# Performance work log

Measured on AMD Instinct MI355X. Metric: run time of the kernel, lower is better.

## Reference

```python
import jax, jax.numpy as jnp
import numpy as np
from jax import lax

D, H, DH, F, K, L, N = 512, 8, 64, 2048, 31, 512, 16
EPS = 1e-5

def layer_norm(x, g, b):
    m = x.mean(-1, keepdims=True)
    v = ((x - m) ** 2).mean(-1, keepdims=True)
    return (x - m) / jnp.sqrt(v + EPS) * g + b

def swish(x):
    return x * jax.nn.sigmoid(x)

def ffn(x, w1, b1, w2, b2):
    return swish(x @ w1.T + b1) @ w2.T + b2

def rel_shift(x):
    # x: (N,H,T,2T-1) -> (N,H,T,T); out[...,i,j] = x[...,i, T-1-i+j]
    T = x.shape[2]
    rows = jnp.arange(T)[:, None]
    cols = (T - 1) - rows + jnp.arange(T)[None, :]
    return x[:, :, rows, cols]

def rel_attn(x, pos_emb, in_w, in_b, out_w, out_b, pos_w, bu, bv):
    Lq, Nb, E = x.shape
    qkv = x @ in_w.T + in_b  # (L,N,3E)
    q, k, v = jnp.split(qkv, 3, axis=-1)
    q = q.reshape(Lq, Nb, H, DH).transpose(1, 2, 0, 3)  # (N,H,L,DH)
    k = k.reshape(Lq, Nb, H, DH).transpose(1, 2, 0, 3)
    v = v.reshape(Lq, Nb, H, DH).transpose(1, 2, 0, 3)
    p = (pos_emb[0] @ pos_w.T).reshape(-1, H, DH).transpose(1, 0, 2)  # (H,2L-1,DH)
    scaling = DH ** -0.5
    q_u = q + bu[None, :, None, :]
    q_v = q + bv[None, :, None, :]
    matrix_ac = jnp.einsum('nhld,nhsd->nhls', q_u, k)        # (N,H,L,L)
    matrix_bd = jnp.einsum('nhld,hmd->nhlm', q_v, p)         # (N,H,L,2L-1)
    matrix_bd = rel_shift(matrix_bd)                         # (N,H,L,L)
    attn = jax.nn.softmax((matrix_ac + matrix_bd) * scaling, axis=-1)
    out = jnp.einsum('nhls,nhsd->nhld', attn, v)
    out = out.transpose(2, 0, 1, 3).reshape(Lq, Nb, E)
    return out @ out_w.T + out_b

def conv_module(x, pw1_w, pw1_b, dw_w, dw_b, g, b, mean, var, pw2_w, pw2_b):
    # x: (L,N,C) -> (N,C,L)
    y = x.transpose(1, 2, 0)
    y = jnp.einsum('ncl,oc->nol', y, pw1_w) + pw1_b[None, :, None]
    a, gate = jnp.split(y, 2, axis=1)
    y = a * jax.nn.sigmoid(gate)  # GLU over channel dim
    pad = (K - 1) // 2
    y = lax.conv_general_dilated(y, dw_w[:, None, :], (1,), [(pad, pad)],
                                 feature_group_count=D,
                                 dimension_numbers=('NCH', 'OIH', 'NCH'))
    y = y + dw_b[None, :, None]
    # BatchNorm1d in eval mode with running stats
    y = (y - mean[None, :, None]) / jnp.sqrt(var[None, :, None] + EPS)
    y = y * g[None, :, None] + b[None, :, None]
    y = swish(y)
    y = jnp.einsum('ncl,oc->nol', y, pw2_w) + pw2_b[None, :, None]
    return y.transpose(2, 0, 1)  # back to (L,N,C)

def setup_inputs() -> dict:
    key = jax.random.key(0)
    ks = iter(jax.random.split(key, 64))
    def nrm(shape, s=0.02):
        return jax.random.normal(next(ks), shape, dtype=jnp.float32) * s
    return {
        'src': jax.random.normal(next(ks), (L, N, D), dtype=jnp.float32),
        'pos_emb': jax.random.normal(next(ks), (1, 2 * L - 1, D), dtype=jnp.float32),
        'ffm_w1': nrm((F, D)), 'ffm_b1': jnp.zeros((F,), jnp.float32),
        'ffm_w2': nrm((D, F)), 'ffm_b2': jnp.zeros((D,), jnp.float32),
        'ff_w1': nrm((F, D)), 'ff_b1': jnp.zeros((F,), jnp.float32),
        'ff_w2': nrm((D, F)), 'ff_b2': jnp.zeros((D,), jnp.float32),
        'in_proj_w': nrm((3 * D, D)), 'in_proj_b': jnp.zeros((3 * D,), jnp.float32),
        'out_proj_w': nrm((D, D)), 'out_proj_b': jnp.zeros((D,), jnp.float32),
        'pos_w': nrm((D, D)),
        'pos_bias_u': nrm((H, DH)), 'pos_bias_v': nrm((H, DH)),
        'conv_pw1_w': nrm((2 * D, D)), 'conv_pw1_b': jnp.zeros((2 * D,), jnp.float32),
        'conv_dw_w': nrm((D, K)), 'conv_dw_b': jnp.zeros((D,), jnp.float32),
        'bn_gamma': jnp.ones((D,), jnp.float32), 'bn_beta': jnp.zeros((D,), jnp.float32),
        'bn_mean': jnp.zeros((D,), jnp.float32), 'bn_var': jnp.ones((D,), jnp.float32),
        'conv_pw2_w': nrm((D, D)), 'conv_pw2_b': jnp.zeros((D,), jnp.float32),
        'ln_ffm_g': jnp.ones((D,), jnp.float32), 'ln_ffm_b': jnp.zeros((D,), jnp.float32),
        'ln_mha_g': jnp.ones((D,), jnp.float32), 'ln_mha_b': jnp.zeros((D,), jnp.float32),
        'ln_conv_g': jnp.ones((D,), jnp.float32), 'ln_conv_b': jnp.zeros((D,), jnp.float32),
        'ln_ff_g': jnp.ones((D,), jnp.float32), 'ln_ff_b': jnp.zeros((D,), jnp.float32),
        'ln_final_g': jnp.ones((D,), jnp.float32), 'ln_final_b': jnp.zeros((D,), jnp.float32),
    }

def reference(src, pos_emb, ffm_w1, ffm_b1, ffm_w2, ffm_b2, ff_w1, ff_b1, ff_w2, ff_b2,
              in_proj_w, in_proj_b, out_proj_w, out_proj_b, pos_w, pos_bias_u, pos_bias_v,
              conv_pw1_w, conv_pw1_b, conv_dw_w, conv_dw_b, bn_gamma, bn_beta, bn_mean, bn_var,
              conv_pw2_w, conv_pw2_b, ln_ffm_g, ln_ffm_b, ln_mha_g, ln_mha_b, ln_conv_g, ln_conv_b,
              ln_ff_g, ln_ff_b, ln_final_g, ln_final_b):
    # pre-norm conformer block, ff_scale = 0.5, dropout omitted (eval)
    x = src
    x = x + 0.5 * ffn(layer_norm(x, ln_ffm_g, ln_ffm_b), ffm_w1, ffm_b1, ffm_w2, ffm_b2)
    x = x + rel_attn(layer_norm(x, ln_mha_g, ln_mha_b), pos_emb,
                     in_proj_w, in_proj_b, out_proj_w, out_proj_b,
                     pos_w, pos_bias_u, pos_bias_v)
    x = x + conv_module(layer_norm(x, ln_conv_g, ln_conv_b),
                        conv_pw1_w, conv_pw1_b, conv_dw_w, conv_dw_b,
                        bn_gamma, bn_beta, bn_mean, bn_var, conv_pw2_w, conv_pw2_b)
    x = x + 0.5 * ffn(layer_norm(x, ln_ff_g, ln_ff_b), ff_w1, ff_b1, ff_w2, ff_b2)
    return layer_norm(x, ln_final_g, ln_final_b)
```

## Files before the change

### kernel.cpp

```cpp
#include <hip/hip_runtime.h>
#include <cstdint>
#include <cstddef>

typedef unsigned short u16;
typedef __attribute__((ext_vector_type(4))) float f32x4;
typedef __attribute__((ext_vector_type(8))) short bf16x8;
typedef __attribute__((ext_vector_type(8))) unsigned short u16x8;

__device__ __forceinline__ float sigm(float x) { return 1.f / (1.f + __expf(-x)); }
__device__ __forceinline__ float bf2f(u16 u) {
    union { unsigned int i; float f; } c; c.i = ((unsigned int)u) << 16; return c.f;
}
__device__ __forceinline__ u16 f2bf(float f) {
    union { float f; unsigned int i; } c; c.f = f;
    unsigned int x = c.i;
    x += 0x7fffu + ((x >> 16) & 1u);
    return (u16)(x >> 16);
}


__global__ void castall_k(const float* __restrict__ s0, const float* __restrict__ s1,
                          const float* __restrict__ s2, const float* __restrict__ s3,
                          const float* __restrict__ s4, const float* __restrict__ s5,
                          const float* __restrict__ s6, const float* __restrict__ s7,
                          const float* __restrict__ s8, const float* __restrict__ s9,
                          u16* __restrict__ dst) {
    int i = blockIdx.x * 256 + threadIdx.x;
    if (i >= 6815232) return;
    const float* s; int off;
    if      (i < 1048576) { s = s0; off = 0; }
    else if (i < 2097152) { s = s1; off = 1048576; }
    else if (i < 3145728) { s = s2; off = 2097152; }
    else if (i < 4194304) { s = s3; off = 3145728; }
    else if (i < 4980736) { s = s4; off = 4194304; }
    else if (i < 5242880) { s = s5; off = 4980736; }
    else if (i < 5767168) { s = s6; off = 5242880; }
    else if (i < 6029312) { s = s7; off = 5767168; }
    else if (i < 6291456) { s = s8; off = 6029312; }
    else                  { s = s9; off = 6291456; }
    dst[i] = f2bf(s[i - off]);
}

template <bool OUTBF>
__global__ __launch_bounds__(256) void ln512_k(const float* __restrict__ x,
                                               const float* __restrict__ g,
                                               const float* __restrict__ b,
                                               void* __restrict__ outv) {
    int row = blockIdx.x * 4 + (threadIdx.x >> 6);
    int lane = threadIdx.x & 63;
    const float* xr = x + (size_t)row * 512 + lane * 8;
    float4 v0 = *(const float4*)(xr);
    float4 v1 = *(const float4*)(xr + 4);
    float va[8] = {v0.x, v0.y, v0.z, v0.w, v1.x, v1.y, v1.z, v1.w};
    float s = 0.f;
#pragma unroll
    for (int t = 0; t < 8; t++) s += va[t];
#pragma unroll
    for (int o = 32; o > 0; o >>= 1) s += __shfl_xor(s, o);
    float m = s * (1.0f / 512.0f);
    float q = 0.f;
#pragma unroll
    for (int t = 0; t < 8; t++) { float d = va[t] - m; q += d * d; }
#pragma unroll
    for (int o = 32; o > 0; o >>= 1) q += __shfl_xor(q, o);
    float inv = rsqrtf(q * (1.0f / 512.0f) + 1e-5f);
    int cb = lane * 8;
    if (OUTBF) {
        u16* o = (u16*)outv + (size_t)row * 512 + cb;
#pragma unroll
        for (int t = 0; t < 8; t++)
            o[t] = f2bf((va[t] - m) * inv * g[cb + t] + b[cb + t]);
    } else {
        float* o = (float*)outv + (size_t)row * 512 + cb;
#pragma unroll
        for (int t = 0; t < 8; t++)
            o[t] = (va[t] - m) * inv * g[cb + t] + b[cb + t];
    }
}

__global__ __launch_bounds__(256) void mgemm_k(
    const u16* __restrict__ A, const u16* __restrict__ B, const float* __restrict__ bias,
    const float* __restrict__ add, void* __restrict__ Cv,
    int M, int Nn, int Kk, float coef, int act, int outbf) {
    __shared__ u16 lA[2][4096];
    __shared__ u16 lB[2][4096];
    int tid = threadIdx.x;
    int lane = tid & 63;
    int w = tid >> 6;
    int wm = (w >> 1) * 64, wn = (w & 1) * 64;
    int m0 = blockIdx.x << 7, n0 = blockIdx.y << 7;

    f32x4 acc[4][4];
#pragma unroll
    for (int i = 0; i < 4; i++)
#pragma unroll
        for (int j = 0; j < 4; j++) acc[i][j] = (f32x4){0.f, 0.f, 0.f, 0.f};

    int srow = tid >> 2;
    int scol = (tid & 3) << 3;
    const u16* gA = A + (size_t)(m0 + srow) * Kk + scol;
    const u16* gB = B + (size_t)(n0 + srow) * Kk + scol;
    int lso = tid * 8;
    int lra = wm * 32 + (lane & 15) * 32 + (lane >> 4) * 8;
    int lrb = wn * 32 + (lane & 15) * 32 + (lane >> 4) * 8;

    auto STAGE = [&](int buf, int k0) {
        __builtin_amdgcn_global_load_lds(
            (const __attribute__((address_space(1))) void*)(gA + k0),
            (__attribute__((address_space(3))) void*)(lA[buf] + lso), 16, 0, 0);
        __builtin_amdgcn_global_load_lds(
            (const __attribute__((address_space(1))) void*)(gA + (size_t)64 * Kk + k0),
            (__attribute__((address_space(3))) void*)(lA[buf] + 2048 + lso), 16, 0, 0);
        __builtin_amdgcn_global_load_lds(
            (const __attribute__((address_space(1))) void*)(gB + k0),
            (__attribute__((address_space(3))) void*)(lB[buf] + lso), 16, 0, 0);
        __builtin_amdgcn_global_load_lds(
            (const __attribute__((address_space(1))) void*)(gB + (size_t)64 * Kk + k0),
            (__attribute__((address_space(3))) void*)(lB[buf] + 2048 + lso), 16, 0, 0);
    };
    auto COMP = [&](int buf) {
        bf16x8 af[4], bf[4];
#pragma unroll
        for (int t = 0; t < 4; t++) {
            af[t] = *(const bf16x8*)(lA[buf] + lra + t * 512);
            bf[t] = *(const bf16x8*)(lB[buf] + lrb + t * 512);
        }
#pragma unroll
        for (int i = 0; i < 4; i++)
#pragma unroll
            for (int j = 0; j < 4; j++)
                acc[i][j] = __builtin_amdgcn_mfma_f32_16x16x32_bf16(af[i], bf[j], acc[i][j], 0, 0, 0);
    };

    int nk = Kk >> 5;
    STAGE(0, 0);
    __syncthreads();
    for (int kt = 1; kt < nk; kt++) {
        STAGE(kt & 1, kt << 5);
        COMP((kt - 1) & 1);
        __syncthreads();
    }
    COMP((nk - 1) & 1);

    int rbase = (lane >> 4) * 4;
    int ncol = lane & 15;
#pragma unroll
    for (int i = 0; i < 4; i++) {
#pragma unroll
        for (int j = 0; j < 4; j++) {
            int n = n0 + wn + j * 16 + ncol;
            float bv = bias ? bias[n] : 0.f;
#pragma unroll
            for (int r = 0; r < 4; r++) {
                int m = m0 + wm + i * 16 + rbase + r;
                float c = acc[i][j][r] + bv;
                if (act == 1) c *= sigm(c);
                size_t o = (size_t)m * Nn + n;
                if (add) c = add[o] + coef * c;
                if (outbf) ((u16*)Cv)[o] = f2bf(c);
                else ((float*)Cv)[o] = c;
            }
        }
    }
}

__global__ __launch_bounds__(256) void posb_k(const u16* __restrict__ A,
                                              const u16* __restrict__ B,
                                              u16* __restrict__ Pbf) {
    __shared__ u16 lA[4096];
    __shared__ u16 lB[4096];
    const int Kk = 512;
    int tid = threadIdx.x;
    int lane = tid & 63, w = tid >> 6;
    int wm = (w >> 1) * 64, wn = (w & 1) * 64;
    int m0 = blockIdx.x << 7, n0 = blockIdx.y << 7;

    f32x4 acc[4][4];
#pragma unroll
    for (int i = 0; i < 4; i++)
#pragma unroll
        for (int j = 0; j < 4; j++) acc[i][j] = (f32x4){0.f, 0.f, 0.f, 0.f};

    int srow = tid >> 2;
    int scol = (tid & 3) << 3;
    int ar0 = m0 + srow;       if (ar0 > 1022) ar0 = 1022;
    int ar1 = m0 + 64 + srow;  if (ar1 > 1022) ar1 = 1022;
    const u16* gA0 = A + (size_t)ar0 * Kk + scol;
    const u16* gA1 = A + (size_t)ar1 * Kk + scol;
    const u16* gB = B + (size_t)(n0 + srow) * Kk + scol;
    int lso = tid * 8;
    int lra = wm * 32 + (lane & 15) * 32 + (lane >> 4) * 8;
    int lrb = wn * 32 + (lane & 15) * 32 + (lane >> 4) * 8;

    for (int k0 = 0; k0 < Kk; k0 += 32) {
        __builtin_amdgcn_global_load_lds(
            (const __attribute__((address_space(1))) void*)(gA0 + k0),
            (__attribute__((address_space(3))) void*)(lA + lso), 16, 0, 0);
        __builtin_amdgcn_global_load_lds(
            (const __attribute__((address_space(1))) void*)(gA1 + k0),
            (__attribute__((address_space(3))) void*)(lA + 2048 + lso), 16, 0, 0);
        __builtin_amdgcn_global_load_lds(
            (const __attribute__((address_space(1))) void*)(gB + k0),
            (__attribute__((address_space(3))) void*)(lB + lso), 16, 0, 0);
        __builtin_amdgcn_global_load_lds(
            (const __attribute__((address_space(1))) void*)(gB + (size_t)64 * Kk + k0),
            (__attribute__((address_space(3))) void*)(lB + 2048 + lso), 16, 0, 0);
        __syncthreads();
        bf16x8 af[4], bf[4];
#pragma unroll
        for (int t = 0; t < 4; t++) {
            af[t] = *(const bf16x8*)(lA + lra + t * 512);
            bf[t] = *(const bf16x8*)(lB + lrb + t * 512);
        }
#pragma unroll
        for (int i = 0; i < 4; i++)
#pragma unroll
            for (int j = 0; j < 4; j++)
                acc[i][j] = __builtin_amdgcn_mfma_f32_16x16x32_bf16(af[i], bf[j], acc[i][j], 0, 0, 0);
        __syncthreads();
    }

    int rbase = (lane >> 4) * 4;
    int ncol = lane & 15;
#pragma unroll
    for (int i = 0; i < 4; i++) {
#pragma unroll
        for (int j = 0; j < 4; j++) {
            int n = n0 + wn + j * 16 + ncol;
            int h = n >> 6, d = n & 63;
#pragma unroll
            for (int r = 0; r < 4; r++) {
                int m = m0 + wm + i * 16 + rbase + r;
                u16 val = (m < 1023) ? f2bf(acc[i][j][r]) : (u16)0;
                Pbf[(((size_t)(h * 1024 + m)) << 6) + d] = val;
            }
        }
    }
}

__global__ __launch_bounds__(256) void fattn_k(
    const u16* __restrict__ QU, const u16* __restrict__ QV,
    const u16* __restrict__ Kb, const u16* __restrict__ Pbf,
    const u16* __restrict__ VT, u16* __restrict__ ctx) {
    __shared__ u16 arr[19072];
    u16* sRect = arr;
    u16* sP = arr;
    u16* sCtx = arr + 16768;
    float* sRed = (float*)(arr + 18816);

    int tid = threadIdx.x;
    int lane = tid & 63, w = tid >> 6;
    int quad = lane >> 4, col = lane & 15;
    int nh = blockIdx.x, h = nh & 7, nb = nh >> 3;
    int m0 = blockIdx.y << 5;
    int nlo = 480 - m0;

    const u16* QVz = QV + ((size_t)nh << 15);
    const u16* QUz = QU + ((size_t)nh << 15);
    const u16* Kz  = Kb + ((size_t)nh << 15);
    const u16* Vz  = VT + ((size_t)nh << 15);
    const u16* Pb  = Pbf + ((size_t)h << 16);

    bf16x8 av[2][2];
#pragma unroll
    for (int ks = 0; ks < 2; ks++)
#pragma unroll
        for (int t = 0; t < 2; t++)
            av[ks][t] = *(const bf16x8*)(QVz + ((size_t)(m0 + t * 16 + col) << 6) + (ks << 5) + quad * 8);
#pragma unroll
    for (int idx = 0; idx < 9; idx++) {
        int nt = w + (idx << 2);
        if (nt < 34) {
            int crow = nt * 16 + col;
            const u16* pb = Pb + ((size_t)(nlo + crow) << 6) + quad * 8;
            f32x4 b0 = (f32x4){0.f, 0.f, 0.f, 0.f};
            f32x4 b1 = (f32x4){0.f, 0.f, 0.f, 0.f};
#pragma unroll
            for (int ks = 0; ks < 2; ks++) {
                bf16x8 bfr = *(const bf16x8*)(pb + (ks << 5));
                b0 = __builtin_amdgcn_mfma_f32_16x16x32_bf16(av[ks][0], bfr, b0, 0, 0, 0);
                b1 = __builtin_amdgcn_mfma_f32_16x16x32_bf16(av[ks][1], bfr, b1, 0, 0, 0);
            }
#pragma unroll
            for (int r = 0; r < 4; r++) {
                int ml0 = quad * 4 + r;
                int j0 = crow + ml0 - 31;
                if (j0 >= 0 && j0 < 512) sRect[ml0 * 524 + j0] = f2bf(b0[r]);
                int ml1 = ml0 + 16;
                int j1 = crow + ml1 - 31;
                if (j1 >= 0 && j1 < 512) sRect[ml1 * 524 + j1] = f2bf(b1[r]);
            }
        }
    }

    bf16x8 au[2][2];
#pragma unroll
    for (int ks = 0; ks < 2; ks++)
#pragma unroll
        for (int t = 0; t < 2; t++)
            au[ks][t] = *(const bf16x8*)(QUz + ((size_t)(m0 + t * 16 + col) << 6) + (ks << 5) + quad * 8);
    f32x4 ac[2][8];
#pragma unroll
    for (int t = 0; t < 2; t++)
#pragma unroll
        for (int jt = 0; jt < 8; jt++) ac[t][jt] = (f32x4){0.f, 0.f, 0.f, 0.f};
#pragma unroll
    for (int jt = 0; jt < 8; jt++) {
        const u16* kp = Kz + ((size_t)((w << 7) + jt * 16 + col) << 6) + quad * 8;
#pragma unroll
        for (int ks = 0; ks < 2; ks++) {
            bf16x8 bfr = *(const bf16x8*)(kp + (ks << 5));
            ac[0][jt] = __builtin_amdgcn_mfma_f32_16x16x32_bf16(au[ks][0], bfr, ac[0][jt], 0, 0, 0);
            ac[1][jt] = __builtin_amdgcn_mfma_f32_16x16x32_bf16(au[ks][1], bfr, ac[1][jt], 0, 0, 0);
        }
    }
    __syncthreads();

    float rmax[2][4];
#pragma unroll
    for (int t = 0; t < 2; t++)
#pragma unroll
        for (int r = 0; r < 4; r++) rmax[t][r] = -1e30f;
#pragma unroll
    for (int jt = 0; jt < 8; jt++) {
        int j = (w << 7) + jt * 16 + col;
#pragma unroll
        for (int t = 0; t < 2; t++)
#pragma unroll
            for (int r = 0; r < 4; r++) {
                int ml = t * 16 + quad * 4 + r;
                float v = (ac[t][jt][r] + bf2f(sRect[ml * 524 + j])) * 0.125f;
                ac[t][jt][r] = v;
                rmax[t][r] = fmaxf(rmax[t][r], v);
            }
    }
#pragma unroll
    for (int o = 1; o <= 8; o <<= 1)
#pragma unroll
        for (int t = 0; t < 2; t++)
#pragma unroll
            for (int r = 0; r < 4; r++) rmax[t][r] = fmaxf(rmax[t][r], __shfl_xor(rmax[t][r], o));
    if (col == 0)
#pragma unroll
        for (int t = 0; t < 2; t++)
#pragma unroll
            for (int r = 0; r < 4; r++) sRed[(t * 16 + quad * 4 + r) * 4 + w] = rmax[t][r];
    __syncthreads();
    float gmax[2][4], psum[2][4];
#pragma unroll
    for (int t = 0; t < 2; t++)
#pragma unroll
        for (int r = 0; r < 4; r++) {
            int ml = t * 16 + quad * 4 + r;
            gmax[t][r] = fmaxf(fmaxf(sRed[ml * 4 + 0], sRed[ml * 4 + 1]),
                               fmaxf(sRed[ml * 4 + 2], sRed[ml * 4 + 3]));
            psum[t][r] = 0.f;
        }
    __syncthreads();
#pragma unroll
    for (int jt = 0; jt < 8; jt++)
#pragma unroll
        for (int t = 0; t < 2; t++)
#pragma unroll
            for (int r = 0; r < 4; r++) {
                float e = __expf(ac[t][jt][r] - gmax[t][r]);
                ac[t][jt][r] = e;
                psum[t][r] += e;
            }
#pragma unroll
    for (int o = 1; o <= 8; o <<= 1)
#pragma unroll
        for (int t = 0; t < 2; t++)
#pragma unroll
            for (int r = 0; r < 4; r++) psum[t][r] += __shfl_xor(psum[t][r], o);
    if (col == 0)
#pragma unroll
        for (int t = 0; t < 2; t++)
#pragma unroll
            for (int r = 0; r < 4; r++) sRed[(t * 16 + quad * 4 + r) * 4 + w] = psum[t][r];
    __syncthreads();
    float rinv[2][4];
#pragma unroll
    for (int t = 0; t < 2; t++)
#pragma unroll
        for (int r = 0; r < 4; r++) {
            int ml = t * 16 + quad * 4 + r;
            rinv[t][r] = 1.f / (sRed[ml * 4 + 0] + sRed[ml * 4 + 1] + sRed[ml * 4 + 2] + sRed[ml * 4 + 3]);
        }

#pragma unroll
    for (int jt = 0; jt < 8; jt++) {
        int j = (w << 7) + jt * 16 + col;
#pragma unroll
        for (int t = 0; t < 2; t++)
#pragma unroll
            for (int r = 0; r < 4; r++)
                sP[(t * 16 + quad * 4 + r) * 520 + j] = f2bf(ac[t][jt][r] * rinv[t][r]);
    }
    __syncthreads();

    f32x4 cacc[2];
    cacc[0] = (f32x4){0.f, 0.f, 0.f, 0.f};
    cacc[1] = (f32x4){0.f, 0.f, 0.f, 0.f};
    {
        const u16* vp = Vz + ((size_t)((w << 4) + col) << 9) + quad * 8;
#pragma unroll
        for (int kc = 0; kc < 2; kc++)
#pragma unroll
            for (int s2 = 0; s2 < 8; s2++) {
                int ko = (kc << 8) + (s2 << 5);
                bf16x8 a0 = *(const bf16x8*)(sP + col * 520 + ko + quad * 8);
                bf16x8 a1 = *(const bf16x8*)(sP + (col + 16) * 520 + ko + quad * 8);
                bf16x8 bfr = *(const bf16x8*)(vp + ko);
                cacc[0] = __builtin_amdgcn_mfma_f32_16x16x32_bf16(a0, bfr, cacc[0], 0, 0, 0);
                cacc[1] = __builtin_amdgcn_mfma_f32_16x16x32_bf16(a1, bfr, cacc[1], 0, 0, 0);
            }
    }

#pragma unroll
    for (int t = 0; t < 2; t++)
#pragma unroll
        for (int r = 0; r < 4; r++)
            sCtx[(t * 16 + quad * 4 + r) * 64 + (w << 4) + col] = f2bf(cacc[t][r]);
    __syncthreads();
    {
        int row = tid >> 3, seg = tid & 7;
        u16* dst = ctx + (((size_t)((m0 + row) * 16 + nb)) << 9) + (h << 6) + seg * 8;
        *(uint4*)dst = *(const uint4*)(sCtx + row * 64 + seg * 8);
    }
}

__global__ __launch_bounds__(256) void repack_k(const u16* __restrict__ qkv,
                                                const float* __restrict__ bu,
                                                const float* __restrict__ bv,
                                                u16* __restrict__ QU, u16* __restrict__ QV,
                                                u16* __restrict__ Kb, u16* __restrict__ VT) {
    __shared__ u16 sV[64 * 72];
    int nh = blockIdx.x, h = nh & 7, n = nh >> 3;
    int l0 = blockIdx.y << 6;
    int tid = threadIdx.x;
    int d8 = (tid & 7) << 3;
    float bub[8], bvb[8];
#pragma unroll
    for (int e = 0; e < 8; e++) {
        bub[e] = bu[h * 64 + d8 + e];
        bvb[e] = bv[h * 64 + d8 + e];
    }
#pragma unroll
    for (int rep = 0; rep < 2; rep++) {
        int ll = (tid >> 3) + rep * 32;
        int l = l0 + ll;
        size_t base = (size_t)(l * 16 + n) * 1536 + h * 64 + d8;
        u16x8 q = *(const u16x8*)(qkv + base);
        u16x8 k = *(const u16x8*)(qkv + base + 512);
        u16x8 v = *(const u16x8*)(qkv + base + 1024);
        u16x8 qu, qv;
#pragma unroll
        for (int e = 0; e < 8; e++) {
            float qf = bf2f(q[e]);
            qu[e] = f2bf(qf + bub[e]);
            qv[e] = f2bf(qf + bvb[e]);
        }
        size_t o = ((size_t)nh * 512 + l) * 64 + d8;
        *(u16x8*)(QU + o) = qu;
        *(u16x8*)(QV + o) = qv;
        *(u16x8*)(Kb + o) = k;
        *(u16x8*)(sV + ll * 72 + d8) = v;
    }
    __syncthreads();
    int d = tid >> 2, ls = (tid & 3) << 4;
    u16 tmp[16];
#pragma unroll
    for (int e = 0; e < 16; e++) tmp[e] = sV[(ls + e) * 72 + d];
    u16* dst = VT + ((size_t)nh * 64 + d) * 512 + l0 + ls;
    *(u16x8*)(dst) = *(const u16x8*)(tmp);
    *(u16x8*)(dst + 8) = *(const u16x8*)(tmp + 8);
}

__global__ void glu_k(const u16* __restrict__ pw1o, u16* __restrict__ g) {
    int e = blockIdx.x * 256 + threadIdx.x;
    int t = e >> 9, c = e & 511;
    float a = bf2f(pw1o[(size_t)t * 1024 + c]);
    float ga = bf2f(pw1o[(size_t)t * 1024 + 512 + c]);
    g[e] = f2bf(a * sigm(ga));
}

__global__ __launch_bounds__(256) void dwconv_k(
    const u16* __restrict__ g, const float* __restrict__ w, const float* __restrict__ wb,
    const float* __restrict__ bng, const float* __restrict__ bnb, const float* __restrict__ bnm,
    const float* __restrict__ bnv, u16* __restrict__ out) {
    int idx = blockIdx.x * 256 + threadIdx.x;
    int c = idx & 511;
    int t = idx >> 9;
    int n = t & 15, l0 = (t >> 4) << 4;
    float win[46];
#pragma unroll
    for (int q = 0; q < 46; q++) {
        int ll = l0 - 15 + q;
        win[q] = (ll >= 0 && ll < 512) ? bf2f(g[((size_t)(ll * 16 + n) << 9) + c]) : 0.f;
    }
    float wgt[31];
#pragma unroll
    for (int k = 0; k < 31; k++) wgt[k] = w[c * 31 + k];
    float ivg = rsqrtf(bnv[c] + 1e-5f) * bng[c];
    float mc = bnm[c], bc = bnb[c], wbc = wb[c];
#pragma unroll
    for (int r = 0; r < 16; r++) {
        float acc = 0.f;
#pragma unroll
        for (int k = 0; k < 31; k++) acc += wgt[k] * win[r + k];
        acc += wbc;
        float y = (acc - mc) * ivg + bc;
        y = y * sigm(y);
        out[((size_t)((l0 + r) * 16 + n) << 9) + c] = f2bf(y);
    }
}

extern "C" void kernel_launch(void* const* d_in, const int* in_sizes, int n_in,
                              void* d_out, int out_size, void* d_ws, size_t ws_size,
                              hipStream_t stream) {
    const float* src      = (const float*)d_in[0];
    const float* pos_emb  = (const float*)d_in[1];
    const float* ffm_w1   = (const float*)d_in[2];
    const float* ffm_b1   = (const float*)d_in[3];
    const float* ffm_w2   = (const float*)d_in[4];
    const float* ffm_b2   = (const float*)d_in[5];
    const float* ff_w1    = (const float*)d_in[6];
    const float* ff_b1    = (const float*)d_in[7];
    const float* ff_w2    = (const float*)d_in[8];
    const float* ff_b2    = (const float*)d_in[9];
    const float* in_w     = (const float*)d_in[10];
    const float* in_b     = (const float*)d_in[11];
    const float* out_w    = (const float*)d_in[12];
    const float* out_b    = (const float*)d_in[13];
    const float* pos_w    = (const float*)d_in[14];
    const float* bu       = (const float*)d_in[15];
    const float* bv       = (const float*)d_in[16];
    const float* pw1_w    = (const float*)d_in[17];
    const float* pw1_b    = (const float*)d_in[18];
    const float* dw_w     = (const float*)d_in[19];
    const float* dw_b     = (const float*)d_in[20];
    const float* bng      = (const float*)d_in[21];
    const float* bnb      = (const float*)d_in[22];
    const float* bnm      = (const float*)d_in[23];
    const float* bnv      = (const float*)d_in[24];
    const float* pw2_w    = (const float*)d_in[25];
    const float* pw2_b    = (const float*)d_in[26];
    const float* ln_ffm_g = (const float*)d_in[27];
    const float* ln_ffm_b = (const float*)d_in[28];
    const float* ln_mha_g = (const float*)d_in[29];
    const float* ln_mha_b = (const float*)d_in[30];
    const float* ln_cv_g  = (const float*)d_in[31];
    const float* ln_cv_b  = (const float*)d_in[32];
    const float* ln_ff_g  = (const float*)d_in[33];
    const float* ln_ff_b  = (const float*)d_in[34];
    const float* ln_fin_g = (const float*)d_in[35];
    const float* ln_fin_b = (const float*)d_in[36];
    (void)in_sizes; (void)n_in; (void)out_size; (void)ws_size;

    const size_t MEG = 1048576;
    u16* U = (u16*)d_ws;
    float* xA = (float*)U;
    u16* Pbf = U;
    float* xB = (float*)(U + 8 * MEG);
    u16* LNB = U + 16 * MEG;
    u16* BIG = U + 20 * MEG;
    u16* QU = U + 36 * MEG;
    u16* QV = U + 40 * MEG;
    u16* Kb = U + 44 * MEG;
    u16* VT = U + 48 * MEG;
    u16* WB = U + 52 * MEG;
    u16* w_ffm1 = WB;
    u16* w_ffm2 = WB + 1 * MEG;
    u16* w_ff1  = WB + 2 * MEG;
    u16* w_ff2  = WB + 3 * MEG;
    u16* w_in   = WB + 4 * MEG;
    u16* w_out  = WB + 4 * MEG + 786432;
    u16* w_pw1  = WB + 5 * MEG;
    u16* w_pw2  = WB + 5 * MEG + 524288;
    u16* w_pos  = WB + 6029312;
    u16* w_pe   = WB + 6291456;
    u16* CTX = LNB;
    u16* GLU = QU;
    u16* CACT = QV;

    castall_k<<<26622, 256, 0, stream>>>(ffm_w1, ffm_w2, ff_w1, ff_w2, in_w, out_w,
                                         pw1_w, pw2_w, pos_w, pos_emb, WB);

    ln512_k<true><<<2048, 256, 0, stream>>>(src, ln_ffm_g, ln_ffm_b, LNB);
    mgemm_k<<<dim3(64, 16), 256, 0, stream>>>(LNB, w_ffm1, ffm_b1, nullptr, BIG,
                                              8192, 2048, 512, 0.f, 1, 1);
    mgemm_k<<<dim3(64, 4), 256, 0, stream>>>(BIG, w_ffm2, ffm_b2, src, xB,
                                             8192, 512, 2048, 0.5f, 0, 0);

    ln512_k<true><<<2048, 256, 0, stream>>>(xB, ln_mha_g, ln_mha_b, LNB);
    posb_k<<<dim3(8, 4), 256, 0, stream>>>(w_pe, w_pos, Pbf);
    mgemm_k<<<dim3(64, 12), 256, 0, stream>>>(LNB, w_in, in_b, nullptr, BIG,
                                              8192, 1536, 512, 0.f, 0, 1);
    repack_k<<<dim3(128, 8), 256, 0, stream>>>(BIG, bu, bv, QU, QV, Kb, VT);
    fattn_k<<<dim3(128, 16), 256, 0, stream>>>(QU, QV, Kb, Pbf, VT, CTX);
    mgemm_k<<<dim3(64, 4), 256, 0, stream>>>(CTX, w_out, out_b, xB, xA,
                                             8192, 512, 512, 1.f, 0, 0);

    ln512_k<true><<<2048, 256, 0, stream>>>(xA, ln_cv_g, ln_cv_b, LNB);
    mgemm_k<<<dim3(64, 8), 256, 0, stream>>>(LNB, w_pw1, pw1_b, nullptr, BIG,
                                             8192, 1024, 512, 0.f, 0, 1);
    glu_k<<<16384, 256, 0, stream>>>(BIG, GLU);
    dwconv_k<<<1024, 256, 0, stream>>>(GLU, dw_w, dw_b, bng, bnb, bnm, bnv, CACT);
    mgemm_k<<<dim3(64, 4), 256, 0, stream>>>(CACT, w_pw2, pw2_b, xA, xB,
                                             8192, 512, 512, 1.f, 0, 0);

    ln512_k<true><<<2048, 256, 0, stream>>>(xB, ln_ff_g, ln_ff_b, LNB);
    mgemm_k<<<dim3(64, 16), 256, 0, stream>>>(LNB, w_ff1, ff_b1, nullptr, BIG,
                                              8192, 2048, 512, 0.f, 1, 1);
    mgemm_k<<<dim3(64, 4), 256, 0, stream>>>(BIG, w_ff2, ff_b2, xB, xA,
                                             8192, 512, 2048, 0.5f, 0, 0);

    ln512_k<false><<<2048, 256, 0, stream>>>(xA, ln_fin_g, ln_fin_b, (float*)d_out);
}
```

Before: 607.5 us.

## Add 256x256-tile GEMM with direct-to-LDS loads for wide projections

Adds a new 512-thread GEMM kernel with 256x256 output tiles, double-buffered 64-wide K slices loaded straight into LDS via global_load_lds with an XOR swizzle, and 16x16x32 bf16 MFMA. It is used for the four wide-N projections (FFN up-projections, QKV in-projection, pointwise conv 1). The larger tile is meant to raise operand reuse and cut global traffic per FLOP. The cost is 128KB of LDS per block and far fewer blocks (128–256 on 256 CUs), which risks low occupancy and poor CU fill.

```diff
diff --git a/kernel.cpp b/kernel.cpp
--- a/kernel.cpp
+++ b/kernel.cpp
@@ -75,6 +75,108 @@
 #pragma unroll
         for (int t = 0; t < 8; t++)
             o[t] = (va[t] - m) * inv * g[cb + t] + b[cb + t];
+    }
+}
+
+__global__ __launch_bounds__(512, 2) void mgemm256_k(
+    const u16* __restrict__ A, const u16* __restrict__ B, const float* __restrict__ bias,
+    const float* __restrict__ add, void* __restrict__ Cv,
+    int M, int Nn, int Kk, float coef, int act, int outbf) {
+    __shared__ u16 sh[65536];
+    int tid = threadIdx.x;
+    int lane = tid & 63, w = tid >> 6;
+    int quad = lane >> 4, rl = lane & 15;
+    int wm = w >> 2, wn = w & 3;
+    int m0 = blockIdx.x << 8, n0 = blockIdx.y << 8;
+    int aw = wm * 128, bw = wn * 64;
+
+    f32x4 acc[8][4];
+#pragma unroll
+    for (int i = 0; i < 8; i++)
+#pragma unroll
+        for (int j = 0; j < 4; j++) acc[i][j] = (f32x4){0.f, 0.f, 0.f, 0.f};
+
+    int srow = tid >> 3;
+    int sxor = (((tid & 7) ^ (srow & 7)) << 3);
+
+    auto STAGE = [&](int tile, int bsel) {
+        int kb = tile << 6;
+        u16* la = sh + (bsel << 14);
+        u16* lb = sh + 32768 + (bsel << 14);
+#pragma unroll
+        for (int i = 0; i < 4; i++) {
+            int r = srow + (i << 6);
+            __builtin_amdgcn_global_load_lds(
+                (const __attribute__((address_space(1))) void*)(A + (size_t)(m0 + r) * Kk + kb + sxor),
+                (__attribute__((address_space(3))) void*)(la + tid * 8 + (i << 12)), 16, 0, 0);
+        }
+#pragma unroll
+        for (int i = 0; i < 4; i++) {
+            int r = srow + (i << 6);
+            __builtin_amdgcn_global_load_lds(
+                (const __attribute__((address_space(1))) void*)(B + (size_t)(n0 + r) * Kk + kb + sxor),
+                (__attribute__((address_space(3))) void*)(lb + tid * 8 + (i << 12)), 16, 0, 0);
+        }
+    };
+
+    auto COMP = [&](int bsel) {
+        const u16* sA = sh + (bsel << 14);
+        const u16* sB = sh + 32768 + (bsel << 14);
+#pragma unroll
+        for (int ks = 0; ks < 2; ks++) {
+            int xoff = ((((ks << 2) + quad) ^ (lane & 7)) << 3);
+            bf16x8 bfr[4];
+#pragma unroll
+            for (int nf = 0; nf < 4; nf++)
+                bfr[nf] = *(const bf16x8*)(sB + (bw + nf * 16 + rl) * 64 + xoff);
+#pragma unroll
+            for (int mf = 0; mf < 8; mf++) {
+                bf16x8 afr = *(const bf16x8*)(sA + (aw + mf * 16 + rl) * 64 + xoff);
+#pragma unroll
+                for (int nf = 0; nf < 4; nf++)
+                    acc[mf][nf] = __builtin_amdgcn_mfma_f32_16x16x32_bf16(afr, bfr[nf], acc[mf][nf], 0, 0, 0);
+            }
+        }
+    };
+
+    int nk = Kk >> 6;
+    STAGE(0, 0);
+    STAGE(1, 1);
+    asm volatile("s_waitcnt vmcnt(8)" ::: "memory");
+    __builtin_amdgcn_s_barrier();
+    int cur = 0;
+    for (int t = 0; t < nk; t++) {
+        COMP(cur);
+        asm volatile("s_waitcnt lgkmcnt(0)" ::: "memory");
+        __builtin_amdgcn_s_barrier();
+        if (t + 2 < nk) {
+            STAGE(t + 2, cur);
+            asm volatile("s_waitcnt vmcnt(8)" ::: "memory");
+        } else if (t == nk - 2) {
+            asm volatile("s_waitcnt vmcnt(0)" ::: "memory");
+        }
+        __builtin_amdgcn_s_barrier();
+        cur ^= 1;
+    }
+
+    int rbase = quad * 4;
+#pragma unroll
+    for (int mf = 0; mf < 8; mf++) {
+#pragma unroll
+        for (int nf = 0; nf < 4; nf++) {
+            int n = n0 + bw + nf * 16 + rl;
+            float bv = bias ? bias[n] : 0.f;
+#pragma unroll
+            for (int r = 0; r < 4; r++) {
+                int m = m0 + aw + mf * 16 + rbase + r;
+                float c = acc[mf][nf][r] + bv;
+                if (act == 1) c *= sigm(c);
+                size_t o = (size_t)m * Nn + n;
+                if (add) c = add[o] + coef * c;
+                if (outbf) ((u16*)Cv)[o] = f2bf(c);
+                else ((float*)Cv)[o] = c;
+            }
+        }
     }
 }
 
@@ -588,31 +690,31 @@
                                          pw1_w, pw2_w, pos_w, pos_emb, WB);
 
     ln512_k<true><<<2048, 256, 0, stream>>>(src, ln_ffm_g, ln_ffm_b, LNB);
-    mgemm_k<<<dim3(64, 16), 256, 0, stream>>>(LNB, w_ffm1, ffm_b1, nullptr, BIG,
-                                              8192, 2048, 512, 0.f, 1, 1);
+    mgemm256_k<<<dim3(32, 8), 512, 0, stream>>>(LNB, w_ffm1, ffm_b1, nullptr, BIG,
+                                                8192, 2048, 512, 0.f, 1, 1);
     mgemm_k<<<dim3(64, 4), 256, 0, stream>>>(BIG, w_ffm2, ffm_b2, src, xB,
                                              8192, 512, 2048, 0.5f, 0, 0);
 
     ln512_k<true><<<2048, 256, 0, stream>>>(xB, ln_mha_g, ln_mha_b, LNB);
     posb_k<<<dim3(8, 4), 256, 0, stream>>>(w_pe, w_pos, Pbf);
-    mgemm_k<<<dim3(64, 12), 256, 0, stream>>>(LNB, w_in, in_b, nullptr, BIG,
-                                              8192, 1536, 512, 0.f, 0, 1);
+    mgemm256_k<<<dim3(32, 6), 512, 0, stream>>>(LNB, w_in, in_b, nullptr, BIG,
+                                                8192, 1536, 512, 0.f, 0, 1);
     repack_k<<<dim3(128, 8), 256, 0, stream>>>(BIG, bu, bv, QU, QV, Kb, VT);
     fattn_k<<<dim3(128, 16), 256, 0, stream>>>(QU, QV, Kb, Pbf, VT, CTX);
     mgemm_k<<<dim3(64, 4), 256, 0, stream>>>(CTX, w_out, out_b, xB, xA,
                                              8192, 512, 512, 1.f, 0, 0);
 
     ln512_k<true><<<2048, 256, 0, stream>>>(xA, ln_cv_g, ln_cv_b, LNB);
-    mgemm_k<<<dim3(64, 8), 256, 0, stream>>>(LNB, w_pw1, pw1_b, nullptr, BIG,
-                                             8192, 1024, 512, 0.f, 0, 1);
+    mgemm256_k<<<dim3(32, 4), 512, 0, stream>>>(LNB, w_pw1, pw1_b, nullptr, BIG,
+                                                8192, 1024, 512, 0.f, 0, 1);
     glu_k<<<16384, 256, 0, stream>>>(BIG, GLU);
     dwconv_k<<<1024, 256, 0, stream>>>(GLU, dw_w, dw_b, bng, bnb, bnm, bnv, CACT);
     mgemm_k<<<dim3(64, 4), 256, 0, stream>>>(CACT, w_pw2, pw2_b, xA, xB,
                                              8192, 512, 512, 1.f, 0, 0);
 
     ln512_k<true><<<2048, 256, 0, stream>>>(xB, ln_ff_g, ln_ff_b, LNB);
-    mgemm_k<<<dim3(64, 16), 256, 0, stream>>>(LNB, w_ff1, ff_b1, nullptr, BIG,
-                                              8192, 2048, 512, 0.f, 1, 1);
+    mgemm256_k<<<dim3(32, 8), 512, 0, stream>>>(LNB, w_ff1, ff_b1, nullptr, BIG,
+                                                8192, 2048, 512, 0.f, 1, 1);
     mgemm_k<<<dim3(64, 4), 256, 0, stream>>>(BIG, w_ff2, ff_b2, xB, xA,
                                              8192, 512, 2048, 0.5f, 0, 0);
 
```

Result: slower. 620.7 us (+2.2%).

## Replace LDS-staged GEMM with single-wave direct-global-load MFMA kernel

Applied to the files above, without the earlier changes.

Swaps the 256-thread, double-buffered LDS GEMM (128x128 tiles) for a 64-thread kernel that computes a 64x64 tile per wave and loads bf16 MFMA fragments directly from global memory. This removes LDS staging and block-level barriers and raises the block count. In exchange it loses shared-memory reuse across waves, has no software prefetch to hide load latency, and increases redundant global/L2 traffic.

```diff
diff --git a/kernel.cpp b/kernel.cpp
--- a/kernel.cpp
+++ b/kernel.cpp
@@ -78,17 +78,13 @@
     }
 }
 
-__global__ __launch_bounds__(256) void mgemm_k(
+__global__ __launch_bounds__(64, 4) void gemm1w_k(
     const u16* __restrict__ A, const u16* __restrict__ B, const float* __restrict__ bias,
     const float* __restrict__ add, void* __restrict__ Cv,
     int M, int Nn, int Kk, float coef, int act, int outbf) {
-    __shared__ u16 lA[2][4096];
-    __shared__ u16 lB[2][4096];
-    int tid = threadIdx.x;
-    int lane = tid & 63;
-    int w = tid >> 6;
-    int wm = (w >> 1) * 64, wn = (w & 1) * 64;
-    int m0 = blockIdx.x << 7, n0 = blockIdx.y << 7;
+    int lane = threadIdx.x;
+    int rl = lane & 15, quad = lane >> 4;
+    int m0 = blockIdx.x << 6, n0 = blockIdx.y << 6;
 
     f32x4 acc[4][4];
 #pragma unroll
@@ -96,63 +92,37 @@
 #pragma unroll
         for (int j = 0; j < 4; j++) acc[i][j] = (f32x4){0.f, 0.f, 0.f, 0.f};
 
-    int srow = tid >> 2;
-    int scol = (tid & 3) << 3;
-    const u16* gA = A + (size_t)(m0 + srow) * Kk + scol;
-    const u16* gB = B + (size_t)(n0 + srow) * Kk + scol;
-    int lso = tid * 8;
-    int lra = wm * 32 + (lane & 15) * 32 + (lane >> 4) * 8;
-    int lrb = wn * 32 + (lane & 15) * 32 + (lane >> 4) * 8;
-
-    auto STAGE = [&](int buf, int k0) {
-        __builtin_amdgcn_global_load_lds(
-            (const __attribute__((address_space(1))) void*)(gA + k0),
-            (__attribute__((address_space(3))) void*)(lA[buf] + lso), 16, 0, 0);
-        __builtin_amdgcn_global_load_lds(
-            (const __attribute__((address_space(1))) void*)(gA + (size_t)64 * Kk + k0),
-            (__attribute__((address_space(3))) void*)(lA[buf] + 2048 + lso), 16, 0, 0);
-        __builtin_amdgcn_global_load_lds(
-            (const __attribute__((address_space(1))) void*)(gB + k0),
-            (__attribute__((address_space(3))) void*)(lB[buf] + lso), 16, 0, 0);
-        __builtin_amdgcn_global_load_lds(
-            (const __attribute__((address_space(1))) void*)(gB + (size_t)64 * Kk + k0),
-            (__attribute__((address_space(3))) void*)(lB[buf] + 2048 + lso), 16, 0, 0);
-    };
-    auto COMP = [&](int buf) {
-        bf16x8 af[4], bf[4];
-#pragma unroll
-        for (int t = 0; t < 4; t++) {
-            af[t] = *(const bf16x8*)(lA[buf] + lra + t * 512);
-            bf[t] = *(const bf16x8*)(lB[buf] + lrb + t * 512);
-        }
+    const u16* pa[4];
+    const u16* pb[4];
+#pragma unroll
+    for (int i = 0; i < 4; i++) {
+        pa[i] = A + (size_t)(m0 + i * 16 + rl) * Kk + quad * 8;
+        pb[i] = B + (size_t)(n0 + i * 16 + rl) * Kk + quad * 8;
+    }
+
+    for (int k0 = 0; k0 < Kk; k0 += 32) {
+        bf16x8 af[4], bfr[4];
+#pragma unroll
+        for (int i = 0; i < 4; i++) af[i] = *(const bf16x8*)(pa[i] + k0);
+#pragma unroll
+        for (int j = 0; j < 4; j++) bfr[j] = *(const bf16x8*)(pb[j] + k0);
 #pragma unroll
         for (int i = 0; i < 4; i++)
 #pragma unroll
             for (int j = 0; j < 4; j++)
-                acc[i][j] = __builtin_amdgcn_mfma_f32_16x16x32_bf16(af[i], bf[j], acc[i][j], 0, 0, 0);
-    };
-
-    int nk = Kk >> 5;
-    STAGE(0, 0);
-    __syncthreads();
-    for (int kt = 1; kt < nk; kt++) {
-        STAGE(kt & 1, kt << 5);
-        COMP((kt - 1) & 1);
-        __syncthreads();
-    }
-    COMP((nk - 1) & 1);
-
-    int rbase = (lane >> 4) * 4;
-    int ncol = lane & 15;
+                acc[i][j] = __builtin_amdgcn_mfma_f32_16x16x32_bf16(af[i], bfr[j], acc[i][j], 0, 0, 0);
+    }
+
+    int rbase = quad * 4;
 #pragma unroll
     for (int i = 0; i < 4; i++) {
 #pragma unroll
         for (int j = 0; j < 4; j++) {
-            int n = n0 + wn + j * 16 + ncol;
+            int n = n0 + j * 16 + rl;
             float bv = bias ? bias[n] : 0.f;
 #pragma unroll
             for (int r = 0; r < 4; r++) {
-                int m = m0 + wm + i * 16 + rbase + r;
+                int m = m0 + i * 16 + rbase + r;
                 float c = acc[i][j][r] + bv;
                 if (act == 1) c *= sigm(c);
                 size_t o = (size_t)m * Nn + n;
@@ -588,33 +558,33 @@
                                          pw1_w, pw2_w, pos_w, pos_emb, WB);
 
     ln512_k<true><<<2048, 256, 0, stream>>>(src, ln_ffm_g, ln_ffm_b, LNB);
-    mgemm_k<<<dim3(64, 16), 256, 0, stream>>>(LNB, w_ffm1, ffm_b1, nullptr, BIG,
-                                              8192, 2048, 512, 0.f, 1, 1);
-    mgemm_k<<<dim3(64, 4), 256, 0, stream>>>(BIG, w_ffm2, ffm_b2, src, xB,
-                                             8192, 512, 2048, 0.5f, 0, 0);
+    gemm1w_k<<<dim3(128, 32), 64, 0, stream>>>(LNB, w_ffm1, ffm_b1, nullptr, BIG,
+                                               8192, 2048, 512, 0.f, 1, 1);
+    gemm1w_k<<<dim3(128, 8), 64, 0, stream>>>(BIG, w_ffm2, ffm_b2, src, xB,
+                                              8192, 512, 2048, 0.5f, 0, 0);
 
     ln512_k<true><<<2048, 256, 0, stream>>>(xB, ln_mha_g, ln_mha_b, LNB);
     posb_k<<<dim3(8, 4), 256, 0, stream>>>(w_pe, w_pos, Pbf);
-    mgemm_k<<<dim3(64, 12), 256, 0, stream>>>(LNB, w_in, in_b, nullptr, BIG,
-                                              8192, 1536, 512, 0.f, 0, 1);
+    gemm1w_k<<<dim3(128, 24), 64, 0, stream>>>(LNB, w_in, in_b, nullptr, BIG,
+                                               8192, 1536, 512, 0.f, 0, 1);
     repack_k<<<dim3(128, 8), 256, 0, stream>>>(BIG, bu, bv, QU, QV, Kb, VT);
     fattn_k<<<dim3(128, 16), 256, 0, stream>>>(QU, QV, Kb, Pbf, VT, CTX);
-    mgemm_k<<<dim3(64, 4), 256, 0, stream>>>(CTX, w_out, out_b, xB, xA,
-                                             8192, 512, 512, 1.f, 0, 0);
+    gemm1w_k<<<dim3(128, 8), 64, 0, stream>>>(CTX, w_out, out_b, xB, xA,
+                                              8192, 512, 512, 1.f, 0, 0);
 
     ln512_k<true><<<2048, 256, 0, stream>>>(xA, ln_cv_g, ln_cv_b, LNB);
-    mgemm_k<<<dim3(64, 8), 256, 0, stream>>>(LNB, w_pw1, pw1_b, nullptr, BIG,
-                                             8192, 1024, 512, 0.f, 0, 1);
+    gemm1w_k<<<dim3(128, 16), 64, 0, stream>>>(LNB, w_pw1, pw1_b, nullptr, BIG,
+                                               8192, 1024, 512, 0.f, 0, 1);
     glu_k<<<16384, 256, 0, stream>>>(BIG, GLU);
     dwconv_k<<<1024, 256, 0, stream>>>(GLU, dw_w, dw_b, bng, bnb, bnm, bnv, CACT);
-    mgemm_k<<<dim3(64, 4), 256, 0, stream>>>(CACT, w_pw2, pw2_b, xA, xB,
-                                             8192, 512, 512, 1.f, 0, 0);
+    gemm1w_k<<<dim3(128, 8), 64, 0, stream>>>(CACT, w_pw2, pw2_b, xA, xB,
+                                              8192, 512, 512, 1.f, 0, 0);
 
     ln512_k<true><<<2048, 256, 0, stream>>>(xB, ln_ff_g, ln_ff_b, LNB);
-    mgemm_k<<<dim3(64, 16), 256, 0, stream>>>(LNB, w_ff1, ff_b1, nullptr, BIG,
-                                              8192, 2048, 512, 0.f, 1, 1);
-    mgemm_k<<<dim3(64, 4), 256, 0, stream>>>(BIG, w_ff2, ff_b2, xB, xA,
-                                             8192, 512, 2048, 0.5f, 0, 0);
+    gemm1w_k<<<dim3(128, 32), 64, 0, stream>>>(LNB, w_ff1, ff_b1, nullptr, BIG,
+                                               8192, 2048, 512, 0.f, 1, 1);
+    gemm1w_k<<<dim3(128, 8), 64, 0, stream>>>(BIG, w_ff2, ff_b2, xB, xA,
+                                              8192, 512, 2048, 0.5f, 0, 0);
 
     ln512_k<false><<<2048, 256, 0, stream>>>(xA, ln_fin_g, ln_fin_b, (float*)d_out);
 }
```

Result: slower. 821.7 us (+35.3%).
